# Kernel optimization log

Hardware: AMD Instinct MI355X
Metric: run time of the kernel (lower is better)

## Reference

```python
import jax, jax.numpy as jnp
import numpy as np
from jax import lax

B, CIN, H, W = 64, 256, 56, 56
WIDTH = 64            # bottleneck width (planes * base_width/64 * groups)
COUT = 256            # planes * expansion
SP_BUDGET = 0.5       # spatial budget
CH_BUDGET = 0.5       # channel budget
K_SP = int(SP_BUDGET * H * W)    # 1568 kept pixels
K_CH = int(CH_BUDGET * WIDTH)    # 32 kept channels
EPS = 1e-5


def _conv(x, w, stride=1, pad=0):
    return lax.conv_general_dilated(
        x, w, (stride, stride), [(pad, pad), (pad, pad)],
        dimension_numbers=('NCHW', 'OIHW', 'NCHW'))


def _bn(x, g, b, m, v):
    scale = g / jnp.sqrt(v + EPS)
    return x * scale[None, :, None, None] + (b - m * scale)[None, :, None, None]


def setup_inputs() -> dict:
    key = jax.random.key(0)
    ks = jax.random.split(key, 6)
    inp = {
        'x': jax.random.normal(ks[0], (B, CIN, H, W), jnp.float32),
        'conv1_w': jax.random.normal(ks[1], (WIDTH, CIN, 1, 1), jnp.float32) * 0.05,
        'bn1_g': jnp.ones((WIDTH,), jnp.float32), 'bn1_b': jnp.zeros((WIDTH,), jnp.float32),
        'bn1_m': jnp.zeros((WIDTH,), jnp.float32), 'bn1_v': jnp.ones((WIDTH,), jnp.float32),
        'conv2_w': jax.random.normal(ks[2], (WIDTH, WIDTH, 3, 3), jnp.float32) * 0.05,
        'bn2_g': jnp.ones((WIDTH,), jnp.float32), 'bn2_b': jnp.zeros((WIDTH,), jnp.float32),
        'bn2_m': jnp.zeros((WIDTH,), jnp.float32), 'bn2_v': jnp.ones((WIDTH,), jnp.float32),
        'conv3_w': jax.random.normal(ks[3], (COUT, WIDTH, 1, 1), jnp.float32) * 0.05,
        'bn3_g': jnp.ones((COUT,), jnp.float32), 'bn3_b': jnp.zeros((COUT,), jnp.float32),
        'bn3_m': jnp.zeros((COUT,), jnp.float32), 'bn3_v': jnp.ones((COUT,), jnp.float32),
        'fc_w': jax.random.normal(ks[4], (WIDTH, CIN), jnp.float32) * 0.05,
        'fc_b': jnp.zeros((WIDTH,), jnp.float32),
        'mask_w': jax.random.normal(ks[5], (1, CIN, 1, 1), jnp.float32) * 0.05,
        'mask_b': jnp.zeros((1,), jnp.float32),
    }
    return inp


def reference(x, conv1_w, bn1_g, bn1_b, bn1_m, bn1_v,
              conv2_w, bn2_g, bn2_b, bn2_m, bn2_v,
              conv3_w, bn3_g, bn3_b, bn3_m, bn3_v,
              fc_w, fc_b, mask_w, mask_b):
    identity = x

    # --- ChannelVectorUnit: pooled fc saliency -> hard channel-budget top-k mask [B, WIDTH]
    pooled = x.mean(axis=(2, 3))                         # [B, CIN]
    ch_sal = jax.nn.sigmoid(pooled @ fc_w.T + fc_b)      # [B, WIDTH]
    ch_kth = lax.top_k(ch_sal, K_CH)[0][:, -1:]          # [B, 1]
    vector = (ch_sal >= ch_kth).astype(x.dtype)          # hard 0/1

    # --- MaskUnit: 1x1-conv spatial saliency -> hard spatial-budget top-k mask [B,1,H,W]
    sp_sal = _conv(x, mask_w) + mask_b[None, :, None, None]   # [B,1,H,W]
    sp_flat = sp_sal.reshape(B, H * W)
    sp_kth = lax.top_k(sp_flat, K_SP)[0][:, -1:]
    mask = (sp_flat >= sp_kth).astype(x.dtype).reshape(B, 1, H, W)
    # dilated mask: 3x3 max-dilation (receptive field of the 3x3 conv)
    mask_dilate = lax.reduce_window(mask, 0.0, lax.max, (1, 1, 3, 3), (1, 1, 1, 1), 'SAME')

    # --- masked bottleneck (dense compute, mask multiplies; stride = 1)
    out = _conv(x, conv1_w)
    out = jax.nn.relu(_bn(out, bn1_g, bn1_b, bn1_m, bn1_v)) * mask_dilate
    out = out * vector[:, :, None, None]                 # channel pruning
    out = _conv(out, conv2_w, stride=1, pad=1)
    out = jax.nn.relu(_bn(out, bn2_g, bn2_b, bn2_m, bn2_v)) * mask
    out = out * vector[:, :, None, None]
    out = _conv(out, conv3_w)
    out = _bn(out, bn3_g, bn3_b, bn3_m, bn3_v) * mask
    out = jax.nn.relu(identity + out)
    return out
```

## Files before the change

kernel.cpp:

```cpp
#include <hip/hip_runtime.h>
#include <math.h>

#define BATCH 64
#define CIN   256
#define HH    56
#define WW    56
#define HW    (HH*WW)
#define WIDTH 64
#define COUT  256
#define K_CH  32
#define K_SP  1568
#define EPS   1e-5f

typedef short short8 __attribute__((ext_vector_type(8)));
typedef float f32x4 __attribute__((ext_vector_type(4)));

#define MFMA16(a, b, c) __builtin_amdgcn_mfma_f32_16x16x32_bf16((a), (b), (c), 0, 0, 0)

__device__ __forceinline__ unsigned short f2bf(float f) {
    unsigned u = __builtin_bit_cast(unsigned, f);
    u += 0x7fffu + ((u >> 16) & 1u);
    return (unsigned short)(u >> 16);
}

__global__ __launch_bounds__(256) void k_prep(const float* __restrict__ w1,
                                              const float* __restrict__ w2,
                                              const float* __restrict__ w3,
                                              short* __restrict__ w1bf,
                                              short* __restrict__ wt2,
                                              short* __restrict__ w3bf) {
    int i = blockIdx.x * 256 + threadIdx.x;
    if (i < 16384) {
        w1bf[i] = (short)f2bf(w1[i]);
    } else if (i < 53248) {
        int j = i - 16384;
        int tap = j >> 12, rem = j & 4095;
        int oc = rem >> 6, c = rem & 63;
        wt2[j] = (short)f2bf(w2[oc * 576 + c * 9 + tap]);
    } else if (i < 69632) {
        int j = i - 53248;
        w3bf[j] = (short)f2bf(w3[j]);
    }
}

__global__ __launch_bounds__(256) void k_poolsal(const float* __restrict__ x,
                                                 const float* __restrict__ mask_w,
                                                 double* __restrict__ pooled,
                                                 double* __restrict__ spart) {
    int ct = blockIdx.x, b = blockIdx.y;
    int tid = threadIdx.x;
    __shared__ double pl[16][257];
    double sp0[4], sp1[4], sp2[4], spt[4];
#pragma unroll
    for (int k = 0; k < 4; k++) { sp0[k] = 0.0; sp1[k] = 0.0; sp2[k] = 0.0; spt[k] = 0.0; }

#pragma clang loop unroll(disable)
    for (int c = 0; c < 16; c++) {
        const float* xr = x + ((size_t)(b * CIN + ct * 16 + c)) * HW;
        double w = (double)mask_w[ct * 16 + c];
        f32x4 v0 = *(const f32x4*)(xr + tid * 4);
        f32x4 v1 = *(const f32x4*)(xr + 1024 + tid * 4);
        f32x4 v2 = *(const f32x4*)(xr + 2048 + tid * 4);
        double s = 0.0;
#pragma unroll
        for (int k = 0; k < 4; k++) {
            double d0 = (double)v0[k], d1 = (double)v1[k], d2 = (double)v2[k];
            sp0[k] += d0 * w; sp1[k] += d1 * w; sp2[k] += d2 * w;
            s += d0 + d1 + d2;
        }
        if (tid < 16) {
            f32x4 v3 = *(const f32x4*)(xr + 3072 + tid * 4);
#pragma unroll
            for (int k = 0; k < 4; k++) {
                double d3 = (double)v3[k];
                spt[k] += d3 * w;
                s += d3;
            }
        }
        pl[c][tid] = s;
    }
    double* so = spart + ((size_t)(b * 16 + ct)) * HW;
#pragma unroll
    for (int k = 0; k < 4; k++) {
        so[tid * 4 + k] = sp0[k];
        so[1024 + tid * 4 + k] = sp1[k];
        so[2048 + tid * 4 + k] = sp2[k];
    }
    if (tid < 16) {
#pragma unroll
        for (int k = 0; k < 4; k++) so[3072 + tid * 4 + k] = spt[k];
    }
    __syncthreads();
    for (int off = 128; off > 0; off >>= 1) {
        for (int k = tid; k < 16 * off; k += 256) {
            int c = k / off, j = k - c * off;
            pl[c][j] += pl[c][j + off];
        }
        __syncthreads();
    }
    if (tid < 16) pooled[b * CIN + ct * 16 + tid] = pl[tid][0] * (1.0 / (double)HW);
}

__global__ __launch_bounds__(256) void k_changather(const double* __restrict__ pooled,
                                                    const float* __restrict__ fc_w,
                                                    const float* __restrict__ fc_b,
                                                    const short* __restrict__ wt2,
                                                    const short* __restrict__ w3bf,
                                                    float* __restrict__ vector,
                                                    int* __restrict__ kidx,
                                                    short* __restrict__ wt2c,
                                                    short* __restrict__ w3c) {
    int b = blockIdx.x, tid = threadIdx.x;
    __shared__ double ps[CIN];
    __shared__ double ss[WIDTH];
    __shared__ double kth;
    __shared__ int ki[K_CH];
    for (int i = tid; i < CIN; i += 256) ps[i] = pooled[b * CIN + i];
    __syncthreads();
    if (tid < 64) {
        double acc = (double)fc_b[tid];
        const float* wr = fc_w + tid * CIN;
        for (int k = 0; k < CIN; k++) acc += ps[k] * (double)wr[k];
        ss[tid] = 1.0 / (1.0 + exp(-acc));
    }
    __syncthreads();
    if (tid < 64) {
        double sal = ss[tid];
        int cg = 0, ce = 0;
        for (int i = 0; i < WIDTH; i++) {
            cg += (ss[i] > sal);
            ce += (ss[i] == sal);
        }
        if (cg <= K_CH - 1 && cg + ce >= K_CH) kth = sal;
    }
    __syncthreads();
    if (tid < 64) {
        double sal = ss[tid];
        int kept = (sal >= kth) ? 1 : 0;
        vector[b * WIDTH + tid] = (float)kept;
        int pos = 0;
        for (int i = 0; i < tid; i++) pos += (ss[i] >= kth) ? 1 : 0;
        if (kept && pos < K_CH) { kidx[b * K_CH + pos] = tid; ki[pos] = tid; }
    }
    __syncthreads();
    for (int i = tid; i < 9216; i += 256) {
        int tap = i >> 10, rem = i & 1023;
        int oc_c = rem >> 5, c_c = rem & 31;
        wt2c[(size_t)b * 9216 + i] = wt2[tap * 4096 + ki[oc_c] * 64 + ki[c_c]];
    }
    for (int i = tid; i < 8192; i += 256) {
        int oc = i >> 5, c_c = i & 31;
        w3c[(size_t)b * 8192 + i] = w3bf[oc * 64 + ki[c_c]];
    }
}

__global__ __launch_bounds__(256) void k_spmask(const double* __restrict__ spart,
                                                float* __restrict__ mask,
                                                float* __restrict__ mdil) {
    int b = blockIdx.x;
    int tid = threadIdx.x;
    __shared__ unsigned long long ks[HW];
    __shared__ float m[HW];
    __shared__ unsigned int hist[256];
    __shared__ unsigned int sc[256];
    __shared__ unsigned long long sh_prefix;
    __shared__ unsigned int sh_krem;

#pragma unroll
    for (int i = 0; i < 13; i++) {
        int px = i * 256 + tid;
        if (px < HW) {
            double s = 0.0;
#pragma unroll
            for (int t = 0; t < 16; t++) s += spart[((size_t)(b * 16 + t)) * HW + px];
            unsigned long long u = __builtin_bit_cast(unsigned long long, s);
            ks[px] = (u >> 63) ? ~u : (u | 0x8000000000000000ULL);
        }
    }
    if (tid == 0) { sh_prefix = 0ULL; sh_krem = K_SP; }
    __syncthreads();

    unsigned long long pmask = 0ULL;
    for (int pass = 0; pass < 8; pass++) {
        int shift = 56 - 8 * pass;
        hist[tid] = 0;
        __syncthreads();
        unsigned long long prefix = sh_prefix;
#pragma unroll
        for (int i = 0; i < 13; i++) {
            int px = i * 256 + tid;
            if (px < HW) {
                unsigned long long k = ks[px];
                if ((k & pmask) == prefix)
                    atomicAdd(&hist[(unsigned)((k >> shift) & 255ULL)], 1u);
            }
        }
        __syncthreads();
        sc[tid] = hist[255 - tid];
        __syncthreads();
        for (int off = 1; off < 256; off <<= 1) {
            unsigned v = sc[tid];
            unsigned a = (tid >= off) ? sc[tid - off] : 0u;
            __syncthreads();
            sc[tid] = v + a;
            __syncthreads();
        }
        unsigned krem = sh_krem;
        unsigned cum = sc[tid];
        unsigned cumHigher = (tid > 0) ? sc[tid - 1] : 0u;
        __syncthreads();
        if (cum >= krem && cumHigher < krem) {
            int d = 255 - tid;
            sh_krem = krem - cumHigher;
            sh_prefix = prefix | ((unsigned long long)d << shift);
        }
        pmask |= (0xFFULL << shift);
        __syncthreads();
    }
    unsigned long long kth = sh_prefix;

#pragma unroll
    for (int i = 0; i < 13; i++) {
        int px = i * 256 + tid;
        if (px < HW) {
            float mv = (ks[px] >= kth) ? 1.0f : 0.0f;
            m[px] = mv;
            mask[b * HW + px] = mv;
        }
    }
    __syncthreads();
    for (int p = tid; p < HW; p += 256) {
        int y = p / WW, xx = p % WW;
        float mx = 0.0f;
        for (int dy = -1; dy <= 1; dy++) {
            int yy = y + dy;
            if (yy < 0 || yy >= HH) continue;
            for (int dx = -1; dx <= 1; dx++) {
                int xc = xx + dx;
                if (xc < 0 || xc >= WW) continue;
                mx = fmaxf(mx, m[yy * WW + xc]);
            }
        }
        mdil[b * HW + p] = mx;
    }
}

__global__ __launch_bounds__(256, 2) void k_conv1(const float* __restrict__ x,
                                                  const short* __restrict__ w1bf,
                                                  const float* __restrict__ g1, const float* __restrict__ b1,
                                                  const float* __restrict__ m1, const float* __restrict__ v1,
                                                  const float* __restrict__ mdil,
                                                  const int* __restrict__ kidx,
                                                  short* __restrict__ out1c) {
    __shared__ float scc[32], shc[32];
    __shared__ int ki[32];
    int b = blockIdx.y, p0 = blockIdx.x * 448;
    int tid = threadIdx.x, w = tid >> 6, lane = tid & 63, g = lane >> 4, ln = lane & 15;
    if (tid < 32) {
        int c = kidx[b * K_CH + tid];
        ki[tid] = c;
        float s = g1[c] * rsqrtf(v1[c] + EPS);
        scc[tid] = s; shc[tid] = b1[c] - m1[c] * s;
    }
    __syncthreads();

    int pxw = p0 + w * 112 + ln;
    f32x4 acc[2][7];
    f32x4 zz = {0.f, 0.f, 0.f, 0.f};
#pragma unroll
    for (int m = 0; m < 2; m++)
#pragma unroll
        for (int nt = 0; nt < 7; nt++) acc[m][nt] = zz;

#pragma unroll
    for (int ks = 0; ks < 8; ks++) {
        short8 afr[2];
#pragma unroll
        for (int m = 0; m < 2; m++)
            afr[m] = *(const short8*)(w1bf + (ki[m * 16 + ln] * 256 + ks * 32 + g * 8));
        const float* xp0 = x + ((size_t)(b * 256 + ks * 32 + g * 8)) * HW + pxw;
#pragma unroll
        for (int nt = 0; nt < 7; nt++) {
            const float* xp = xp0 + nt * 16;
            short8 bfr;
#pragma unroll
            for (int j = 0; j < 8; j++)
                bfr[j] = (short)f2bf(xp[(size_t)j * HW]);
#pragma unroll
            for (int m = 0; m < 2; m++) acc[m][nt] = MFMA16(afr[m], bfr, acc[m][nt]);
        }
    }
#pragma unroll
    for (int nt = 0; nt < 7; nt++) {
        int px = pxw + nt * 16;
        float md = mdil[b * HW + px];
#pragma unroll
        for (int m = 0; m < 2; m++) {
            int oc = m * 16 + g * 4;
            float y0 = fmaxf(acc[m][nt][0] * scc[oc + 0] + shc[oc + 0], 0.f) * md;
            float y1 = fmaxf(acc[m][nt][1] * scc[oc + 1] + shc[oc + 1], 0.f) * md;
            float y2 = fmaxf(acc[m][nt][2] * scc[oc + 2] + shc[oc + 2], 0.f) * md;
            float y3 = fmaxf(acc[m][nt][3] * scc[oc + 3] + shc[oc + 3], 0.f) * md;
            uint2 u;
            u.x = (unsigned)f2bf(y0) | ((unsigned)f2bf(y1) << 16);
            u.y = (unsigned)f2bf(y2) | ((unsigned)f2bf(y3) << 16);
            *(uint2*)(out1c + ((size_t)(b * HW + px)) * 32 + oc) = u;
        }
    }
}

__global__ __launch_bounds__(256, 3) void k_conv2(const short* __restrict__ out1c,
                                                  const short* __restrict__ wt2c,
                                                  const float* __restrict__ g2, const float* __restrict__ b2,
                                                  const float* __restrict__ m2, const float* __restrict__ v2,
                                                  const float* __restrict__ mask,
                                                  const int* __restrict__ kidx,
                                                  short* __restrict__ out2c) {
    __shared__ short lds[10 * 58 * 32];
    __shared__ float scc[32], shc[32];
    int b = blockIdx.y, r0 = blockIdx.x * 8, p0 = r0 * 56;
    int tid = threadIdx.x, w = tid >> 6, lane = tid & 63, g = lane >> 4, ln = lane & 15;
    if (tid < 32) {
        int c = kidx[b * K_CH + tid];
        float s = g2[c] * rsqrtf(v2[c] + EPS);
        scc[tid] = s; shc[tid] = b2[c] - m2[c] * s;
    }
    short8 z8 = {0, 0, 0, 0, 0, 0, 0, 0};
    for (int i = tid; i < 2320; i += 256) {
        int cblk = i & 3;
        int colr = i >> 2;
        int col = colr % 58, ri = colr / 58;
        int gr = r0 - 1 + ri, gc = col - 1;
        short8 v8 = z8;
        if (gr >= 0 && gr < HH && gc >= 0 && gc < WW)
            v8 = *(const short8*)(out1c + ((size_t)(b * HW + gr * WW + gc)) * 32 + cblk * 8);
        *(short8*)(&lds[(ri * 58 + col) * 32 + ((cblk * 8) ^ ((col & 3) << 3))]) = v8;
    }
    __syncthreads();

    f32x4 acc[2][7];
    f32x4 zz = {0.f, 0.f, 0.f, 0.f};
#pragma unroll
    for (int m = 0; m < 2; m++)
#pragma unroll
        for (int nt = 0; nt < 7; nt++) acc[m][nt] = zz;

    const short* wtb = wt2c + (size_t)b * 9216;
    int prel0 = w * 112 + ln;
    for (int tap = 0; tap < 9; tap++) {
        int dy = tap / 3 - 1;
        int dx = tap - (tap / 3) * 3 - 1;
        short8 afr[2];
#pragma unroll
        for (int m = 0; m < 2; m++)
            afr[m] = *(const short8*)(wtb + tap * 1024 + (m * 16 + ln) * 32 + g * 8);
#pragma unroll
        for (int nt = 0; nt < 7; nt++) {
            int prel = prel0 + nt * 16;
            int rrel = prel / 56;
            int xcol = prel - rrel * 56;
            int row_l = rrel + 1 + dy;
            int col_l = xcol + 1 + dx;
            short8 bfr = *(const short8*)(&lds[(row_l * 58 + col_l) * 32 + ((g * 8) ^ ((col_l & 3) << 3))]);
#pragma unroll
            for (int m = 0; m < 2; m++) acc[m][nt] = MFMA16(afr[m], bfr, acc[m][nt]);
        }
    }
#pragma unroll
    for (int nt = 0; nt < 7; nt++) {
        int px = p0 + prel0 + nt * 16;
        float mv = mask[b * HW + px];
#pragma unroll
        for (int m = 0; m < 2; m++) {
            int oc = m * 16 + g * 4;
            float y0 = fmaxf(acc[m][nt][0] * scc[oc + 0] + shc[oc + 0], 0.f) * mv;
            float y1 = fmaxf(acc[m][nt][1] * scc[oc + 1] + shc[oc + 1], 0.f) * mv;
            float y2 = fmaxf(acc[m][nt][2] * scc[oc + 2] + shc[oc + 2], 0.f) * mv;
            float y3 = fmaxf(acc[m][nt][3] * scc[oc + 3] + shc[oc + 3], 0.f) * mv;
            uint2 u;
            u.x = (unsigned)f2bf(y0) | ((unsigned)f2bf(y1) << 16);
            u.y = (unsigned)f2bf(y2) | ((unsigned)f2bf(y3) << 16);
            *(uint2*)(out2c + ((size_t)(b * HW + px)) * 32 + oc) = u;
        }
    }
}

__global__ __launch_bounds__(256, 4) void k_conv3(const short* __restrict__ out2c,
                                                  const short* __restrict__ w3c,
                                                  const float* __restrict__ g3, const float* __restrict__ b3,
                                                  const float* __restrict__ m3, const float* __restrict__ v3,
                                                  const float* __restrict__ mask,
                                                  const float* __restrict__ x,
                                                  float* __restrict__ out) {
    int b = blockIdx.y;
    int ocb = blockIdx.x / 28;
    int pxb = blockIdx.x % 28;
    int p0 = pxb * 112;
    int tid = threadIdx.x, w = tid >> 6, lane = tid & 63, g = lane >> 4, ln = lane & 15;
    int oc0 = ocb * 64 + w * 16;
    int oc = oc0 + ln;

    const short* w3b = w3c + (size_t)b * 8192;
    short8 wfr = *(const short8*)(w3b + oc * 32 + g * 8);

    short8 act[7];
#pragma unroll
    for (int nt = 0; nt < 7; nt++)
        act[nt] = *(const short8*)(out2c + ((size_t)(b * HW + p0 + nt * 16 + ln)) * 32 + g * 8);

    f32x4 xr[7];
#pragma unroll
    for (int nt = 0; nt < 7; nt++) {
        int px0 = p0 + nt * 16 + g * 4;
        xr[nt] = *(const f32x4*)(x + ((size_t)(b * COUT + oc)) * HW + px0);
    }
    __builtin_amdgcn_sched_barrier(0);

    f32x4 acc[7];
    f32x4 zz = {0.f, 0.f, 0.f, 0.f};
#pragma unroll
    for (int nt = 0; nt < 7; nt++) acc[nt] = zz;
#pragma unroll
    for (int nt = 0; nt < 7; nt++)
        acc[nt] = MFMA16(act[nt], wfr, acc[nt]);

    float s_ = g3[oc] * rsqrtf(v3[oc] + EPS);
    float h_ = b3[oc] - m3[oc] * s_;
#pragma unroll
    for (int nt = 0; nt < 7; nt++) {
        int px0 = p0 + nt * 16 + g * 4;
        f32x4 mv = *(const f32x4*)(mask + (size_t)b * HW + px0);
        size_t idx = ((size_t)(b * COUT + oc)) * HW + px0;
        f32x4 o;
#pragma unroll
        for (int i = 0; i < 4; i++)
            o[i] = fmaxf(xr[nt][i] + (acc[nt][i] * s_ + h_) * mv[i], 0.f);
        *(f32x4*)(out + idx) = o;
    }
}

extern "C" void kernel_launch(void* const* d_in, const int* in_sizes, int n_in,
                              void* d_out, int out_size, void* d_ws, size_t ws_size,
                              hipStream_t stream) {
    const float* x       = (const float*)d_in[0];
    const float* conv1_w = (const float*)d_in[1];
    const float* bn1_g   = (const float*)d_in[2];
    const float* bn1_b   = (const float*)d_in[3];
    const float* bn1_m   = (const float*)d_in[4];
    const float* bn1_v   = (const float*)d_in[5];
    const float* conv2_w = (const float*)d_in[6];
    const float* bn2_g   = (const float*)d_in[7];
    const float* bn2_b   = (const float*)d_in[8];
    const float* bn2_m   = (const float*)d_in[9];
    const float* bn2_v   = (const float*)d_in[10];
    const float* conv3_w = (const float*)d_in[11];
    const float* bn3_g   = (const float*)d_in[12];
    const float* bn3_b   = (const float*)d_in[13];
    const float* bn3_m   = (const float*)d_in[14];
    const float* bn3_v   = (const float*)d_in[15];
    const float* fc_w    = (const float*)d_in[16];
    const float* fc_b    = (const float*)d_in[17];
    const float* mask_w  = (const float*)d_in[18];
    const float* mask_b  = (const float*)d_in[19];
    (void)mask_b;

    char* wsb = (char*)d_ws;
    size_t off = 0;
    double* pooled = (double*)(wsb + off); off += (size_t)BATCH * CIN * 8;
    double* spart  = (double*)(wsb + off); off += (size_t)BATCH * 16 * HW * 8;
    float* vector  = (float*)(wsb + off);  off += (size_t)BATCH * WIDTH * 4;
    float* mask    = (float*)(wsb + off);  off += (size_t)BATCH * HW * 4;
    float* mdil    = (float*)(wsb + off);  off += (size_t)BATCH * HW * 4;
    int*   kidx    = (int*)(wsb + off);    off += (size_t)BATCH * K_CH * 4;
    short* w1bf    = (short*)(wsb + off);  off += (size_t)WIDTH * CIN * 2;
    short* wt2     = (short*)(wsb + off);  off += (size_t)9 * WIDTH * WIDTH * 2;
    short* w3bf    = (short*)(wsb + off);  off += (size_t)COUT * WIDTH * 2;
    short* wt2c    = (short*)(wsb + off);  off += (size_t)BATCH * 9216 * 2;
    short* w3c     = (short*)(wsb + off);  off += (size_t)BATCH * 8192 * 2;
    short* out1c   = (short*)(wsb + off);  off += (size_t)BATCH * HW * 32 * 2;
    short* out2c   = (short*)(wsb + off);  off += (size_t)BATCH * HW * 32 * 2;
    (void)ws_size; (void)in_sizes; (void)n_in; (void)out_size; (void)vector;

    k_prep<<<272, 256, 0, stream>>>(conv1_w, conv2_w, conv3_w, w1bf, wt2, w3bf);
    k_poolsal<<<dim3(16, BATCH), 256, 0, stream>>>(x, mask_w, pooled, spart);
    k_changather<<<BATCH, 256, 0, stream>>>(pooled, fc_w, fc_b, wt2, w3bf, vector, kidx, wt2c, w3c);
    k_spmask<<<BATCH, 256, 0, stream>>>(spart, mask, mdil);
    k_conv1<<<dim3(7, BATCH), 256, 0, stream>>>(x, w1bf, bn1_g, bn1_b, bn1_m, bn1_v, mdil, kidx, out1c);
    k_conv2<<<dim3(7, BATCH), 256, 0, stream>>>(out1c, wt2c, bn2_g, bn2_b, bn2_m, bn2_v, mask, kidx, out2c);
    k_conv3<<<dim3(112, BATCH), 256, 0, stream>>>(out2c, w3c, bn3_g, bn3_b, bn3_m, bn3_v, mask, x, (float*)d_out);
}
```

Before: 238.6 us.

## Fuse weight prep into selection kernels, merge channel/spatial select, retile conv2

Drops the separate weight bf16-conversion kernel, so conv1 converts fp32 weights inline and the channel-gather converts w2/w3 directly. Merges the channel-selection and spatial top-k kernels into one launch with block roles, cutting launch count and letting both run concurrently. Retiles conv2 to 4-row tiles with 128-thread blocks and twice the grid, trading more halo reloads for better occupancy. Conv1 now repeats the fp32-to-bf16 conversion in every block, which adds ALU and load work. The conv2 body is hidden, so wave/row mapping consistency with 128 threads is unverified.

Result: faster. 215.4 us (-9.7%).

```diff
diff --git a/kernel.cpp b/kernel.cpp
--- a/kernel.cpp
+++ b/kernel.cpp
@@ -23,26 +23,6 @@
     return (unsigned short)(u >> 16);
 }
 
-__global__ __launch_bounds__(256) void k_prep(const float* __restrict__ w1,
-                                              const float* __restrict__ w2,
-                                              const float* __restrict__ w3,
-                                              short* __restrict__ w1bf,
-                                              short* __restrict__ wt2,
-                                              short* __restrict__ w3bf) {
-    int i = blockIdx.x * 256 + threadIdx.x;
-    if (i < 16384) {
-        w1bf[i] = (short)f2bf(w1[i]);
-    } else if (i < 53248) {
-        int j = i - 16384;
-        int tap = j >> 12, rem = j & 4095;
-        int oc = rem >> 6, c = rem & 63;
-        wt2[j] = (short)f2bf(w2[oc * 576 + c * 9 + tap]);
-    } else if (i < 69632) {
-        int j = i - 53248;
-        w3bf[j] = (short)f2bf(w3[j]);
-    }
-}
-
 __global__ __launch_bounds__(256) void k_poolsal(const float* __restrict__ x,
                                                  const float* __restrict__ mask_w,
                                                  double* __restrict__ pooled,
@@ -101,70 +81,73 @@
     if (tid < 16) pooled[b * CIN + ct * 16 + tid] = pl[tid][0] * (1.0 / (double)HW);
 }
 
-__global__ __launch_bounds__(256) void k_changather(const double* __restrict__ pooled,
-                                                    const float* __restrict__ fc_w,
-                                                    const float* __restrict__ fc_b,
-                                                    const short* __restrict__ wt2,
-                                                    const short* __restrict__ w3bf,
-                                                    float* __restrict__ vector,
-                                                    int* __restrict__ kidx,
-                                                    short* __restrict__ wt2c,
-                                                    short* __restrict__ w3c) {
-    int b = blockIdx.x, tid = threadIdx.x;
-    __shared__ double ps[CIN];
-    __shared__ double ss[WIDTH];
-    __shared__ double kth;
-    __shared__ int ki[K_CH];
-    for (int i = tid; i < CIN; i += 256) ps[i] = pooled[b * CIN + i];
-    __syncthreads();
-    if (tid < 64) {
-        double acc = (double)fc_b[tid];
-        const float* wr = fc_w + tid * CIN;
-        for (int k = 0; k < CIN; k++) acc += ps[k] * (double)wr[k];
-        ss[tid] = 1.0 / (1.0 + exp(-acc));
-    }
-    __syncthreads();
-    if (tid < 64) {
-        double sal = ss[tid];
-        int cg = 0, ce = 0;
-        for (int i = 0; i < WIDTH; i++) {
-            cg += (ss[i] > sal);
-            ce += (ss[i] == sal);
-        }
-        if (cg <= K_CH - 1 && cg + ce >= K_CH) kth = sal;
-    }
-    __syncthreads();
-    if (tid < 64) {
-        double sal = ss[tid];
-        int kept = (sal >= kth) ? 1 : 0;
-        vector[b * WIDTH + tid] = (float)kept;
-        int pos = 0;
-        for (int i = 0; i < tid; i++) pos += (ss[i] >= kth) ? 1 : 0;
-        if (kept && pos < K_CH) { kidx[b * K_CH + pos] = tid; ki[pos] = tid; }
-    }
-    __syncthreads();
-    for (int i = tid; i < 9216; i += 256) {
-        int tap = i >> 10, rem = i & 1023;
-        int oc_c = rem >> 5, c_c = rem & 31;
-        wt2c[(size_t)b * 9216 + i] = wt2[tap * 4096 + ki[oc_c] * 64 + ki[c_c]];
-    }
-    for (int i = tid; i < 8192; i += 256) {
-        int oc = i >> 5, c_c = i & 31;
-        w3c[(size_t)b * 8192 + i] = w3bf[oc * 64 + ki[c_c]];
-    }
-}
-
-__global__ __launch_bounds__(256) void k_spmask(const double* __restrict__ spart,
-                                                float* __restrict__ mask,
-                                                float* __restrict__ mdil) {
-    int b = blockIdx.x;
+__global__ __launch_bounds__(256) void k_sel(const double* __restrict__ pooled,
+                                             const float* __restrict__ fc_w,
+                                             const float* __restrict__ fc_b,
+                                             const float* __restrict__ w2,
+                                             const float* __restrict__ w3,
+                                             const double* __restrict__ spart,
+                                             float* __restrict__ vector,
+                                             int* __restrict__ kidx,
+                                             short* __restrict__ wt2c,
+                                             short* __restrict__ w3c,
+                                             float* __restrict__ mask,
+                                             float* __restrict__ mdil) {
+    int role = blockIdx.x >> 6;
+    int b = blockIdx.x & 63;
     int tid = threadIdx.x;
+
     __shared__ unsigned long long ks[HW];
     __shared__ float m[HW];
     __shared__ unsigned int hist[256];
     __shared__ unsigned int sc[256];
     __shared__ unsigned long long sh_prefix;
     __shared__ unsigned int sh_krem;
+    __shared__ double ps[CIN];
+    __shared__ double ss[WIDTH];
+    __shared__ double kth;
+    __shared__ int ki[K_CH];
+
+    if (role == 1) {
+        for (int i = tid; i < CIN; i += 256) ps[i] = pooled[b * CIN + i];
+        __syncthreads();
+        if (tid < 64) {
+            double acc = (double)fc_b[tid];
+            const float* wr = fc_w + tid * CIN;
+            for (int k = 0; k < CIN; k++) acc += ps[k] * (double)wr[k];
+            ss[tid] = 1.0 / (1.0 + exp(-acc));
+        }
+        __syncthreads();
+        if (tid < 64) {
+            double sal = ss[tid];
+            int cg = 0, ce = 0;
+            for (int i = 0; i < WIDTH; i++) {
+                cg += (ss[i] > sal);
+                ce += (ss[i] == sal);
+            }
+            if (cg <= K_CH - 1 && cg + ce >= K_CH) kth = sal;
+        }
+        __syncthreads();
+        if (tid < 64) {
+            double sal = ss[tid];
+            int kept = (sal >= kth) ? 1 : 0;
+            vector[b * WIDTH + tid] = (float)kept;
+            int pos = 0;
+            for (int i = 0; i < tid; i++) pos += (ss[i] >= kth) ? 1 : 0;
+            if (kept && pos < K_CH) { kidx[b * K_CH + pos] = tid; ki[pos] = tid; }
+        }
+        __syncthreads();
+        for (int i = tid; i < 9216; i += 256) {
+            int tap = i >> 10, rem = i & 1023;
+            int oc_c = rem >> 5, c_c = rem & 31;
+            wt2c[(size_t)b * 9216 + i] = (short)f2bf(w2[ki[oc_c] * 576 + ki[c_c] * 9 + tap]);
+        }
+        for (int i = tid; i < 8192; i += 256) {
+            int oc = i >> 5, c_c = i & 31;
+            w3c[(size_t)b * 8192 + i] = (short)f2bf(w3[oc * 64 + ki[c_c]]);
+        }
+        return;
+    }
 
 #pragma unroll
     for (int i = 0; i < 13; i++) {
@@ -217,13 +200,13 @@
         pmask |= (0xFFULL << shift);
         __syncthreads();
     }
-    unsigned long long kth = sh_prefix;
+    unsigned long long kthk = sh_prefix;
 
 #pragma unroll
     for (int i = 0; i < 13; i++) {
         int px = i * 256 + tid;
         if (px < HW) {
-            float mv = (ks[px] >= kth) ? 1.0f : 0.0f;
+            float mv = (ks[px] >= kthk) ? 1.0f : 0.0f;
             m[px] = mv;
             mask[b * HW + px] = mv;
         }
@@ -246,7 +229,7 @@
 }
 
 __global__ __launch_bounds__(256, 2) void k_conv1(const float* __restrict__ x,
-                                                  const short* __restrict__ w1bf,
+                                                  const float* __restrict__ w1,
                                                   const float* __restrict__ g1, const float* __restrict__ b1,
                                                   const float* __restrict__ m1, const float* __restrict__ v1,
                                                   const float* __restrict__ mdil,
@@ -276,8 +259,16 @@
     for (int ks = 0; ks < 8; ks++) {
         short8 afr[2];
 #pragma unroll
-        for (int m = 0; m < 2; m++)
-            afr[m] = *(const short8*)(w1bf + (ki[m * 16 + ln] * 256 + ks * 32 + g * 8));
+        for (int m = 0; m < 2; m++) {
+            const float* wp = w1 + (ki[m * 16 + ln] * 256 + ks * 32 + g * 8);
+            f32x4 a0 = *(const f32x4*)(wp);
+            f32x4 a1 = *(const f32x4*)(wp + 4);
+#pragma unroll
+            for (int j = 0; j < 4; j++) {
+                afr[m][j]     = (short)f2bf(a0[j]);
+                afr[m][4 + j] = (short)f2bf(a1[j]);
+            }
+        }
         const float* xp0 = x + ((size_t)(b * 256 + ks * 32 + g * 8)) * HW + pxw;
 #pragma unroll
         for (int nt = 0; nt < 7; nt++) {
@@ -309,16 +300,16 @@
     }
 }
 
-__global__ __launch_bounds__(256, 3) void k_conv2(const short* __restrict__ out1c,
+__global__ __launch_bounds__(128, 2) void k_conv2(const short* __restrict__ out1c,
                                                   const short* __restrict__ wt2c,
                                                   const float* __restrict__ g2, const float* __restrict__ b2,
                                                   const float* __restrict__ m2, const float* __restrict__ v2,
                                                   const float* __restrict__ mask,
                                                   const int* __restrict__ kidx,
                                                   short* __restrict__ out2c) {
-    __shared__ short lds[10 * 58 * 32];
+    __shared__ short lds[6 * 58 * 32];
     __shared__ float scc[32], shc[32];
-    int b = blockIdx.y, r0 = blockIdx.x * 8, p0 = r0 * 56;
+    int b = blockIdx.y, r0 = blockIdx.x * 4, p0 = r0 * 56;
     int tid = threadIdx.x, w = tid >> 6, lane = tid & 63, g = lane >> 4, ln = lane & 15;
     if (tid < 32) {
         int c = kidx[b * K_CH + tid];
@@ -326,7 +317,7 @@
         scc[tid] = s; shc[tid] = b2[c] - m2[c] * s;
     }
     short8 z8 = {0, 0, 0, 0, 0, 0, 0, 0};
-    for (int i = tid; i < 2320; i += 256) {
+    for (int i = tid; i < 1392; i += 128) {
         int cblk = i & 3;
         int colr = i >> 2;
         int col = colr % 58, ri = colr / 58;
@@ -472,20 +463,16 @@
     float* mask    = (float*)(wsb + off);  off += (size_t)BATCH * HW * 4;
     float* mdil    = (float*)(wsb + off);  off += (size_t)BATCH * HW * 4;
     int*   kidx    = (int*)(wsb + off);    off += (size_t)BATCH * K_CH * 4;
-    short* w1bf    = (short*)(wsb + off);  off += (size_t)WIDTH * CIN * 2;
-    short* wt2     = (short*)(wsb + off);  off += (size_t)9 * WIDTH * WIDTH * 2;
-    short* w3bf    = (short*)(wsb + off);  off += (size_t)COUT * WIDTH * 2;
     short* wt2c    = (short*)(wsb + off);  off += (size_t)BATCH * 9216 * 2;
     short* w3c     = (short*)(wsb + off);  off += (size_t)BATCH * 8192 * 2;
     short* out1c   = (short*)(wsb + off);  off += (size_t)BATCH * HW * 32 * 2;
     short* out2c   = (short*)(wsb + off);  off += (size_t)BATCH * HW * 32 * 2;
     (void)ws_size; (void)in_sizes; (void)n_in; (void)out_size; (void)vector;
 
-    k_prep<<<272, 256, 0, stream>>>(conv1_w, conv2_w, conv3_w, w1bf, wt2, w3bf);
     k_poolsal<<<dim3(16, BATCH), 256, 0, stream>>>(x, mask_w, pooled, spart);
-    k_changather<<<BATCH, 256, 0, stream>>>(pooled, fc_w, fc_b, wt2, w3bf, vector, kidx, wt2c, w3c);
-    k_spmask<<<BATCH, 256, 0, stream>>>(spart, mask, mdil);
-    k_conv1<<<dim3(7, BATCH), 256, 0, stream>>>(x, w1bf, bn1_g, bn1_b, bn1_m, bn1_v, mdil, kidx, out1c);
-    k_conv2<<<dim3(7, BATCH), 256, 0, stream>>>(out1c, wt2c, bn2_g, bn2_b, bn2_m, bn2_v, mask, kidx, out2c);
+    k_sel<<<128, 256, 0, stream>>>(pooled, fc_w, fc_b, conv2_w, conv3_w, spart,
+                                   vector, kidx, wt2c, w3c, mask, mdil);
+    k_conv1<<<dim3(7, BATCH), 256, 0, stream>>>(x, conv1_w, bn1_g, bn1_b, bn1_m, bn1_v, mdil, kidx, out1c);
+    k_conv2<<<dim3(14, BATCH), 128, 0, stream>>>(out1c, wt2c, bn2_g, bn2_b, bn2_m, bn2_v, mask, kidx, out2c);
     k_conv3<<<dim3(112, BATCH), 256, 0, stream>>>(out2c, w3c, bn3_g, bn3_b, bn3_m, bn3_v, mask, x, (float*)d_out);
 }
```
